# Kernel optimization log

Measured on AMD Instinct MI355X. Metric: run time of the kernel, lower is better.

Reference implementation:

```python
import jax, jax.numpy as jnp
import numpy as np

CODEBOOK_DIM = 12          # log2(codebook_size)
CODEBOOK_SIZE = 4096
DIM = 512
INV_TEMPERATURE = 100.0
CODEBOOK_SCALE = 1.0
DIVERSITY_GAMMA = 1.0
ENTROPY_LOSS_WEIGHT = 0.1
EPS = 1e-5


def setup_inputs() -> dict:
    key = jax.random.key(0)
    k_x, k_wi, k_wo = jax.random.split(key, 3)
    x = jax.random.normal(k_x, (4, 4096, DIM), dtype=jnp.float32)
    # nn.Linear weights: (out_features, in_features)
    w_in = jax.random.normal(k_wi, (CODEBOOK_DIM, DIM), dtype=jnp.float32) * 0.02
    b_in = jnp.zeros((CODEBOOK_DIM,), dtype=jnp.float32)
    w_out = jax.random.normal(k_wo, (DIM, CODEBOOK_DIM), dtype=jnp.float32) * 0.02
    b_out = jnp.zeros((DIM,), dtype=jnp.float32)
    return {"x": x, "w_in": w_in, "b_in": b_in, "w_out": w_out, "b_out": b_out}


def _entropy(prob):
    return (-prob * jnp.log(jnp.clip(prob, EPS))).sum(axis=-1)


def _make_codebook():
    mask = (2 ** jnp.arange(CODEBOOK_DIM - 1, -1, -1)).astype(jnp.int32)  # [d]
    all_codes = jnp.arange(CODEBOOK_SIZE, dtype=jnp.int32)
    bits = ((all_codes[:, None] & mask) != 0).astype(jnp.float32)  # [cs, d]
    codebook = bits * CODEBOOK_SCALE * 2 - CODEBOOK_SCALE  # {-1, +1}
    return mask, codebook


def reference(x, w_in, b_in, w_out, b_out):
    mask, codebook = _make_codebook()

    # project in: [b, n, dim] -> [b, n, d]
    xp = jnp.einsum('bnd,cd->bnc', x, w_in) + b_in  # c == codebook_dim here

    # sign quantization (num_codebooks = 1, so c-dim is implicit)
    quantized = jnp.where(xp > 0, CODEBOOK_SCALE, -CODEBOOK_SCALE).astype(xp.dtype)
    indices = ((quantized > 0).astype(jnp.int32) * mask).sum(axis=-1)  # [b, n]

    # straight-through estimator (training path)
    x_st = xp + jax.lax.stop_gradient(quantized - xp)

    # entropy aux loss over full codebook (frac_per_sample_entropy = 1.0)
    flat = xp.reshape(-1, CODEBOOK_DIM)  # original (pre-quant) input, [bn, d]
    # -distance * inv_temp = 2 * inv_temp * <x, code>
    logits = (2.0 * INV_TEMPERATURE) * (flat @ codebook.T)  # [bn, cs]
    prob = jax.nn.softmax(logits, axis=-1)
    per_sample_entropy = _entropy(prob).mean()
    avg_prob = prob.mean(axis=0)  # [cs]
    codebook_entropy = _entropy(avg_prob)
    entropy_aux_loss = per_sample_entropy - DIVERSITY_GAMMA * codebook_entropy
    aux_loss = entropy_aux_loss * ENTROPY_LOSS_WEIGHT

    # project out: [b, n, d] -> [b, n, dim]
    out = jnp.einsum('bnc,dc->bnd', x_st, w_out) + b_out
    return out, indices, aux_loss
```

## Files before the change

### kernel.cpp

```cpp
#include <hip/hip_runtime.h>
#include <hip/hip_bf16.h>


#define NS    16384
#define NOUT  (NS*512)
#define AUXO  (NOUT+NS)
#define INVT2 200.0f
#define NBLK  512

__global__ __launch_bounds__(512, 4) void k_main(
    const float* __restrict__ x,
    const float* __restrict__ w_in,  const float* __restrict__ b_in,
    const float* __restrict__ w_out, const float* __restrict__ b_out,
    float* __restrict__ out, float* __restrict__ idx_out,
    float* __restrict__ P, float* __restrict__ Csum) {

  __shared__ float s_wi[6144];
  __shared__ float s_wt[6144];
  __shared__ float s_phi[32][64];
  __shared__ float s_psi[32][64];
  __shared__ float s_xp[8][4][12];
  __shared__ float s_h[8];

  const int t = threadIdx.x;

  for (int k = 0; k < 12; ++k) {
    int f  = t + k * 512;
    int kk = f & 3;
    int q  = f >> 2;
    int sub = q & 15, e4 = (q >> 4) & 7, d = q >> 7;
    int e  = sub * 32 + e4 * 4 + kk;
    s_wi[f] = w_in[d * 512 + e];
    s_wt[f] = w_out[t * 12 + k];
  }
  __syncthreads();

  const int wave = t >> 6, lane = t & 63;
  const int g = lane >> 4, sub = lane & 15;

  float bin[12];
  #pragma unroll
  for (int d = 0; d < 12; ++d) bin[d] = b_in[d];

  const int i0 = blockIdx.x * 32 + wave * 4 + g;

  const float4* xr0 = (const float4*)(x + (size_t)i0 * 512 + sub * 32);
  float4 xv0[8];
  #pragma unroll
  for (int e4 = 0; e4 < 8; ++e4) xv0[e4] = xr0[e4];

  float p0[12];
  #pragma unroll
  for (int d = 0; d < 12; ++d) p0[d] = 0.f;
  #pragma unroll
  for (int e4 = 0; e4 < 8; ++e4) {
    #pragma unroll
    for (int d = 0; d < 12; ++d) {
      float4 w4 = ((const float4*)s_wi)[d * 128 + e4 * 16 + sub];
      p0[d] += xv0[e4].x * w4.x + xv0[e4].y * w4.y + xv0[e4].z * w4.z + xv0[e4].w * w4.w;
    }
  }
  #pragma unroll
  for (int d = 0; d < 12; ++d) {
    #pragma unroll
    for (int m = 1; m <= 8; m <<= 1) {
      p0[d] += __shfl_xor(p0[d], m, 16);
    }
    p0[d] += bin[d];
  }

  unsigned idx0 = 0u;
  #pragma unroll
  for (int d = 0; d < 12; ++d) {
    idx0 |= (p0[d] > 0.f ? 1u : 0u) << (11 - d);
  }
  if (sub == 0) {
    idx_out[i0] = (float)idx0;
    #pragma unroll
    for (int d = 0; d < 12; ++d) s_xp[wave][g][d] = p0[d];
  }

  float sg0[12];
  #pragma unroll
  for (int d = 0; d < 12; ++d) sg0[d] = p0[d] > 0.f ? 1.f : -1.f;

  float4* or0 = (float4*)(out + (size_t)i0 * 512);
  #pragma unroll
  for (int e4 = 0; e4 < 8; ++e4) {
    float4 bo = ((const float4*)b_out)[e4 * 16 + sub];
    float4 o0 = bo;
    #pragma unroll
    for (int d = 0; d < 12; ++d) {
      float4 w4 = ((const float4*)s_wt)[d * 128 + e4 * 16 + sub];
      o0.x += sg0[d] * w4.x; o0.y += sg0[d] * w4.y; o0.z += sg0[d] * w4.z; o0.w += sg0[d] * w4.w;
    }
    or0[e4 * 16 + sub] = o0;
  }

  float hacc = 0.f;
  #pragma unroll 1
  for (int s = 0; s < 4; ++s) {
    float xq[12];
    #pragma unroll
    for (int d = 0; d < 12; ++d) xq[d] = s_xp[wave][s][d];

    float hi = 0.f, lo = 0.f, ah = 0.f, al = 0.f;
    #pragma unroll
    for (int d = 0; d < 6; ++d) {
      int bh = (lane >> (5 - d)) & 1;
      hi += bh ? xq[d]     : -xq[d];
      lo += bh ? xq[6 + d] : -xq[6 + d];
      ah += fabsf(xq[d]);
      al += fabsf(xq[6 + d]);
    }
    float lhi = INVT2 * (hi - ah);
    float llo = INVT2 * (lo - al);
    float ehi = __expf(lhi);
    float elo = __expf(llo);
    float Shi = ehi, Slo = elo;
    #pragma unroll
    for (int m = 1; m <= 32; m <<= 1) {
      Shi += __shfl_xor(Shi, m);
      Slo += __shfl_xor(Slo, m);
    }
    float phi = ehi / Shi;
    float psi = elo / Slo;
    float lnShi = __logf(Shi), lnSlo = __logf(Slo);
    hacc += phi * (lhi - lnShi) + psi * (llo - lnSlo);

    const int ws = wave * 4 + s;
    s_phi[ws][lane] = phi;
    s_psi[ws][lane] = psi;
  }

  #pragma unroll
  for (int m = 1; m <= 32; m <<= 1) hacc += __shfl_xor(hacc, m);
  if (lane == 0) s_h[wave] = hacc;
  __syncthreads();
  if (t == 0) {
    float hs = 0.f;
    for (int w2 = 0; w2 < 8; ++w2) hs += s_h[w2];
    atomicAdd(Csum, hs);
  }

  const int jb = (t >> 5) * 4;
  const int lb = (t & 31) * 2;
  float a00 = 0.f, a01 = 0.f, a10 = 0.f, a11 = 0.f;
  float a20 = 0.f, a21 = 0.f, a30 = 0.f, a31 = 0.f;
  #pragma unroll 4
  for (int s = 0; s < 32; ++s) {
    float4 ph = *(const float4*)&s_phi[s][jb];
    float2 ps = *(const float2*)&s_psi[s][lb];
    a00 += ph.x * ps.x; a01 += ph.x * ps.y;
    a10 += ph.y * ps.x; a11 += ph.y * ps.y;
    a20 += ph.z * ps.x; a21 += ph.z * ps.y;
    a30 += ph.w * ps.x; a31 += ph.w * ps.y;
  }
  float* Pr = P + (size_t)blockIdx.x * 4096;
  *(float2*)&Pr[(jb + 0) * 64 + lb] = make_float2(a00, a01);
  *(float2*)&Pr[(jb + 1) * 64 + lb] = make_float2(a10, a11);
  *(float2*)&Pr[(jb + 2) * 64 + lb] = make_float2(a20, a21);
  *(float2*)&Pr[(jb + 3) * 64 + lb] = make_float2(a30, a31);
}

__global__ __launch_bounds__(256) void k_reduce(const float* __restrict__ P,
                                                float* __restrict__ Esum) {
  __shared__ float red[16][17];
  __shared__ float ered[16];
  const int t = threadIdx.x;
  const int cl = t & 15, rg = t >> 4;
  const int c = blockIdx.x * 16 + cl;
  float s = 0.f;
  #pragma unroll
  for (int k = 0; k < 32; ++k) s += P[(size_t)(rg + k * 16) * 4096 + c];
  red[rg][cl] = s;
  __syncthreads();
  if (t < 16) {
    float tot = 0.f;
    #pragma unroll
    for (int r = 0; r < 16; ++r) tot += red[r][t];
    float pb = tot * (1.f / (float)NS);
    ered[t] = pb * __logf(fmaxf(pb, 1e-5f));
  }
  __syncthreads();
  if (t == 0) {
    float e = 0.f;
    #pragma unroll
    for (int r = 0; r < 16; ++r) e += ered[r];
    atomicAdd(Esum, e);
  }
}

__global__ void k_final(const float* __restrict__ Csum, const float* __restrict__ Esum,
                        float* __restrict__ aux) {
  if (threadIdx.x == 0) {
    float per_sample_entropy = -Csum[0] * (1.f / (float)NS);
    float codebook_entropy   = -Esum[0];
    aux[0] = 0.1f * (per_sample_entropy - codebook_entropy);
  }
}

extern "C" void kernel_launch(void* const* d_in, const int* in_sizes, int n_in,
                              void* d_out, int out_size, void* d_ws, size_t ws_size,
                              hipStream_t stream) {
  const float* x     = (const float*)d_in[0];
  const float* w_in  = (const float*)d_in[1];
  const float* b_in  = (const float*)d_in[2];
  const float* w_out = (const float*)d_in[3];
  const float* b_out = (const float*)d_in[4];
  float* out = (float*)d_out;

  float* P    = (float*)d_ws;
  float* scal = (float*)((char*)d_ws + (size_t)NBLK * 4096 * 4);

  hipMemsetAsync(scal, 0, 2 * sizeof(float), stream);
  k_main<<<NBLK, 512, 0, stream>>>(x, w_in, b_in, w_out, b_out,
                                   out, out + NOUT, P, scal);
  k_reduce<<<256, 256, 0, stream>>>(P, scal + 1);
  k_final<<<1, 64, 0, stream>>>(scal, scal + 1, out + AUXO);
}
```

Measured before the change: 113.9 us.

## Precompute 4096-code output table and gather rows; fold final kernel into reduce

Because the straight-through output depends only on the 12 sign bits, a new kernel builds a 4096x512 table of w_out·sign(code)+b_out, and the main kernel copies the row for each token's index instead of doing the 12-term FMA projection. This also drops the shared-memory w_out staging from the main kernel, freeing LDS. Separately, the final aux-loss kernel is folded into the reduce kernel through a last-block counter. The cost is an 8 MB table write plus gathered reads, which may or may not stay in cache, and one extra launch.

```diff
diff --git a/kernel.cpp b/kernel.cpp
--- a/kernel.cpp
+++ b/kernel.cpp
@@ -8,15 +8,43 @@
 #define INVT2 200.0f
 #define NBLK  512
 
+__global__ __launch_bounds__(512) void k_table(const float* __restrict__ w_out,
+                                               const float* __restrict__ b_out,
+                                               float* __restrict__ T) {
+  __shared__ float s_wt[6144];
+  const int t = threadIdx.x;
+  #pragma unroll
+  for (int k = 0; k < 12; ++k) s_wt[t + k * 512] = w_out[t * 12 + k];
+  __syncthreads();
+
+  const int c = blockIdx.x * 16 + (t >> 5);
+  float sg[12];
+  #pragma unroll
+  for (int d = 0; d < 12; ++d) sg[d] = ((c >> (11 - d)) & 1) ? 1.f : -1.f;
+
+  float4* Trow = (float4*)(T + (size_t)c * 512);
+  #pragma unroll
+  for (int k4 = 0; k4 < 4; ++k4) {
+    const int m = (t & 31) + k4 * 32;
+    float4 bo = ((const float4*)b_out)[m];
+    float4 o = bo;
+    #pragma unroll
+    for (int d = 0; d < 12; ++d) {
+      float4 w4 = ((const float4*)s_wt)[d * 128 + m];
+      o.x += sg[d] * w4.x; o.y += sg[d] * w4.y; o.z += sg[d] * w4.z; o.w += sg[d] * w4.w;
+    }
+    Trow[m] = o;
+  }
+}
+
 __global__ __launch_bounds__(512, 4) void k_main(
     const float* __restrict__ x,
     const float* __restrict__ w_in,  const float* __restrict__ b_in,
-    const float* __restrict__ w_out, const float* __restrict__ b_out,
+    const float* __restrict__ T,
     float* __restrict__ out, float* __restrict__ idx_out,
     float* __restrict__ P, float* __restrict__ Csum) {
 
   __shared__ float s_wi[6144];
-  __shared__ float s_wt[6144];
   __shared__ float s_phi[32][64];
   __shared__ float s_psi[32][64];
   __shared__ float s_xp[8][4][12];
@@ -24,6 +52,7 @@
 
   const int t = threadIdx.x;
 
+  #pragma unroll
   for (int k = 0; k < 12; ++k) {
     int f  = t + k * 512;
     int kk = f & 3;
@@ -31,7 +60,6 @@
     int sub = q & 15, e4 = (q >> 4) & 7, d = q >> 7;
     int e  = sub * 32 + e4 * 4 + kk;
     s_wi[f] = w_in[d * 512 + e];
-    s_wt[f] = w_out[t * 12 + k];
   }
   __syncthreads();
 
@@ -80,21 +108,13 @@
     for (int d = 0; d < 12; ++d) s_xp[wave][g][d] = p0[d];
   }
 
-  float sg0[12];
-  #pragma unroll
-  for (int d = 0; d < 12; ++d) sg0[d] = p0[d] > 0.f ? 1.f : -1.f;
-
-  float4* or0 = (float4*)(out + (size_t)i0 * 512);
-  #pragma unroll
-  for (int e4 = 0; e4 < 8; ++e4) {
-    float4 bo = ((const float4*)b_out)[e4 * 16 + sub];
-    float4 o0 = bo;
-    #pragma unroll
-    for (int d = 0; d < 12; ++d) {
-      float4 w4 = ((const float4*)s_wt)[d * 128 + e4 * 16 + sub];
-      o0.x += sg0[d] * w4.x; o0.y += sg0[d] * w4.y; o0.z += sg0[d] * w4.z; o0.w += sg0[d] * w4.w;
-    }
-    or0[e4 * 16 + sub] = o0;
+  {
+    const float4* Trow = (const float4*)(T + (size_t)idx0 * 512);
+    float4* or0 = (float4*)(out + (size_t)i0 * 512);
+    #pragma unroll
+    for (int e4 = 0; e4 < 8; ++e4) {
+      or0[e4 * 16 + sub] = Trow[e4 * 16 + sub];
+    }
   }
 
   float hacc = 0.f;
@@ -164,7 +184,8 @@
 }
 
 __global__ __launch_bounds__(256) void k_reduce(const float* __restrict__ P,
-                                                float* __restrict__ Esum) {
+                                                float* __restrict__ scal,
+                                                float* __restrict__ aux) {
   __shared__ float red[16][17];
   __shared__ float ered[16];
   const int t = threadIdx.x;
@@ -187,16 +208,16 @@
     float e = 0.f;
     #pragma unroll
     for (int r = 0; r < 16; ++r) e += ered[r];
-    atomicAdd(Esum, e);
-  }
-}
-
-__global__ void k_final(const float* __restrict__ Csum, const float* __restrict__ Esum,
-                        float* __restrict__ aux) {
-  if (threadIdx.x == 0) {
-    float per_sample_entropy = -Csum[0] * (1.f / (float)NS);
-    float codebook_entropy   = -Esum[0];
-    aux[0] = 0.1f * (per_sample_entropy - codebook_entropy);
+    atomicAdd(&scal[1], e);
+    __threadfence();
+    unsigned done = atomicAdd((unsigned*)&scal[2], 1u);
+    if (done == 255u) {
+      float E = atomicAdd(&scal[1], 0.f);
+      float C = atomicAdd(&scal[0], 0.f);
+      float per_sample_entropy = -C * (1.f / (float)NS);
+      float codebook_entropy   = -E;
+      aux[0] = 0.1f * (per_sample_entropy - codebook_entropy);
+    }
   }
 }
 
@@ -210,12 +231,13 @@
   const float* b_out = (const float*)d_in[4];
   float* out = (float*)d_out;
 
-  float* P    = (float*)d_ws;
-  float* scal = (float*)((char*)d_ws + (size_t)NBLK * 4096 * 4);
-
-  hipMemsetAsync(scal, 0, 2 * sizeof(float), stream);
-  k_main<<<NBLK, 512, 0, stream>>>(x, w_in, b_in, w_out, b_out,
+  float* T    = (float*)d_ws;
+  float* P    = T + (size_t)4096 * 512;
+  float* scal = P + (size_t)NBLK * 4096;
+
+  hipMemsetAsync(scal, 0, 3 * sizeof(float), stream);
+  k_table<<<256, 512, 0, stream>>>(w_out, b_out, T);
+  k_main<<<NBLK, 512, 0, stream>>>(x, w_in, b_in, T,
                                    out, out + NOUT, P, scal);
-  k_reduce<<<256, 256, 0, stream>>>(P, scal + 1);
-  k_final<<<1, 64, 0, stream>>>(scal, scal + 1, out + AUXO);
-}
+  k_reduce<<<256, 256, 0, stream>>>(P, scal, out + AUXO);
+}
```

Measured after the change: 120.2 us. 1.06x slower.

## Read weights directly from global/L1 instead of LDS staging; fold final kernel into reduce

Applied to the files above, without the earlier changes.

Drops the per-block LDS staging of w_in and w_out (48 KB of shared memory) and the block barrier that follows it. Weights are now read directly from global memory through cache, with the output projection restructured to read w_out rows as contiguous float4s. The lower shared memory use could raise occupancy, but every thread now issues more global and L1 loads. Separately, k_final is removed: the last k_reduce block, found with an atomic counter, computes aux, which saves one kernel launch.

```diff
diff --git a/kernel.cpp b/kernel.cpp
--- a/kernel.cpp
+++ b/kernel.cpp
@@ -15,29 +15,19 @@
     float* __restrict__ out, float* __restrict__ idx_out,
     float* __restrict__ P, float* __restrict__ Csum) {
 
-  __shared__ float s_wi[6144];
-  __shared__ float s_wt[6144];
   __shared__ float s_phi[32][64];
   __shared__ float s_psi[32][64];
   __shared__ float s_xp[8][4][12];
   __shared__ float s_h[8];
 
   const int t = threadIdx.x;
-
-  for (int k = 0; k < 12; ++k) {
-    int f  = t + k * 512;
-    int kk = f & 3;
-    int q  = f >> 2;
-    int sub = q & 15, e4 = (q >> 4) & 7, d = q >> 7;
-    int e  = sub * 32 + e4 * 4 + kk;
-    s_wi[f] = w_in[d * 512 + e];
-    s_wt[f] = w_out[t * 12 + k];
-  }
-  __syncthreads();
-
   const int wave = t >> 6, lane = t & 63;
   const int g = lane >> 4, sub = lane & 15;
 
+  const float4* wi4 = (const float4*)w_in;
+  const float4* wo4 = (const float4*)w_out;
+  const float4* bo4 = (const float4*)b_out;
+
   float bin[12];
   #pragma unroll
   for (int d = 0; d < 12; ++d) bin[d] = b_in[d];
@@ -56,7 +46,7 @@
   for (int e4 = 0; e4 < 8; ++e4) {
     #pragma unroll
     for (int d = 0; d < 12; ++d) {
-      float4 w4 = ((const float4*)s_wi)[d * 128 + e4 * 16 + sub];
+      float4 w4 = wi4[d * 128 + sub * 8 + e4];
       p0[d] += xv0[e4].x * w4.x + xv0[e4].y * w4.y + xv0[e4].z * w4.z + xv0[e4].w * w4.w;
     }
   }
@@ -87,14 +77,34 @@
   float4* or0 = (float4*)(out + (size_t)i0 * 512);
   #pragma unroll
   for (int e4 = 0; e4 < 8; ++e4) {
-    float4 bo = ((const float4*)b_out)[e4 * 16 + sub];
-    float4 o0 = bo;
-    #pragma unroll
-    for (int d = 0; d < 12; ++d) {
-      float4 w4 = ((const float4*)s_wt)[d * 128 + e4 * 16 + sub];
-      o0.x += sg0[d] * w4.x; o0.y += sg0[d] * w4.y; o0.z += sg0[d] * w4.z; o0.w += sg0[d] * w4.w;
-    }
-    or0[e4 * 16 + sub] = o0;
+    const int M = e4 * 16 + sub;
+    const float4* wr = wo4 + 12 * M;
+    float4 o = bo4[M];
+    {
+      float4 a = wr[0], b = wr[1], c = wr[2];
+      o.x += sg0[0]*a.x; o.x += sg0[1]*a.y; o.x += sg0[2]*a.z; o.x += sg0[3]*a.w;
+      o.x += sg0[4]*b.x; o.x += sg0[5]*b.y; o.x += sg0[6]*b.z; o.x += sg0[7]*b.w;
+      o.x += sg0[8]*c.x; o.x += sg0[9]*c.y; o.x += sg0[10]*c.z; o.x += sg0[11]*c.w;
+    }
+    {
+      float4 a = wr[3], b = wr[4], c = wr[5];
+      o.y += sg0[0]*a.x; o.y += sg0[1]*a.y; o.y += sg0[2]*a.z; o.y += sg0[3]*a.w;
+      o.y += sg0[4]*b.x; o.y += sg0[5]*b.y; o.y += sg0[6]*b.z; o.y += sg0[7]*b.w;
+      o.y += sg0[8]*c.x; o.y += sg0[9]*c.y; o.y += sg0[10]*c.z; o.y += sg0[11]*c.w;
+    }
+    {
+      float4 a = wr[6], b = wr[7], c = wr[8];
+      o.z += sg0[0]*a.x; o.z += sg0[1]*a.y; o.z += sg0[2]*a.z; o.z += sg0[3]*a.w;
+      o.z += sg0[4]*b.x; o.z += sg0[5]*b.y; o.z += sg0[6]*b.z; o.z += sg0[7]*b.w;
+      o.z += sg0[8]*c.x; o.z += sg0[9]*c.y; o.z += sg0[10]*c.z; o.z += sg0[11]*c.w;
+    }
+    {
+      float4 a = wr[9], b = wr[10], c = wr[11];
+      o.w += sg0[0]*a.x; o.w += sg0[1]*a.y; o.w += sg0[2]*a.z; o.w += sg0[3]*a.w;
+      o.w += sg0[4]*b.x; o.w += sg0[5]*b.y; o.w += sg0[6]*b.z; o.w += sg0[7]*b.w;
+      o.w += sg0[8]*c.x; o.w += sg0[9]*c.y; o.w += sg0[10]*c.z; o.w += sg0[11]*c.w;
+    }
+    or0[M] = o;
   }
 
   float hacc = 0.f;
@@ -164,7 +174,8 @@
 }
 
 __global__ __launch_bounds__(256) void k_reduce(const float* __restrict__ P,
-                                                float* __restrict__ Esum) {
+                                                float* __restrict__ scal,
+                                                float* __restrict__ aux) {
   __shared__ float red[16][17];
   __shared__ float ered[16];
   const int t = threadIdx.x;
@@ -187,16 +198,16 @@
     float e = 0.f;
     #pragma unroll
     for (int r = 0; r < 16; ++r) e += ered[r];
-    atomicAdd(Esum, e);
-  }
-}
-
-__global__ void k_final(const float* __restrict__ Csum, const float* __restrict__ Esum,
-                        float* __restrict__ aux) {
-  if (threadIdx.x == 0) {
-    float per_sample_entropy = -Csum[0] * (1.f / (float)NS);
-    float codebook_entropy   = -Esum[0];
-    aux[0] = 0.1f * (per_sample_entropy - codebook_entropy);
+    atomicAdd(&scal[1], e);
+    __threadfence();
+    unsigned done = atomicAdd((unsigned*)&scal[2], 1u);
+    if (done == 255u) {
+      float E = atomicAdd(&scal[1], 0.f);
+      float C = atomicAdd(&scal[0], 0.f);
+      float per_sample_entropy = -C * (1.f / (float)NS);
+      float codebook_entropy   = -E;
+      aux[0] = 0.1f * (per_sample_entropy - codebook_entropy);
+    }
   }
 }
 
@@ -211,11 +222,10 @@
   float* out = (float*)d_out;
 
   float* P    = (float*)d_ws;
-  float* scal = (float*)((char*)d_ws + (size_t)NBLK * 4096 * 4);
-
-  hipMemsetAsync(scal, 0, 2 * sizeof(float), stream);
+  float* scal = P + (size_t)NBLK * 4096;
+
+  hipMemsetAsync(scal, 0, 3 * sizeof(float), stream);
   k_main<<<NBLK, 512, 0, stream>>>(x, w_in, b_in, w_out, b_out,
                                    out, out + NOUT, P, scal);
-  k_reduce<<<256, 256, 0, stream>>>(P, scal + 1);
-  k_final<<<1, 64, 0, stream>>>(scal, scal + 1, out + AUXO);
+  k_reduce<<<256, 256, 0, stream>>>(P, scal, out + AUXO);
 }
```

Result: slower. 177.7 us (+56.0%).

## Drop memset and final kernel; fold finalisation into reduce via last-block counter

Applied to the files above, without the earlier changes.

Removes the hipMemsetAsync and the single-thread final kernel. Block 0 of the main kernel now zeroes the scalars, per-block entropy partials are written to a buffer instead of atomics, and the reduce kernel (now 64 blocks with 64 columns each) sums them. The last reduce block, found through an atomic counter, computes the aux loss. This saves two launches per call, at the cost of fewer, longer reduce blocks and an atomic completion protocol.

```diff
diff --git a/kernel.cpp b/kernel.cpp
--- a/kernel.cpp
+++ b/kernel.cpp
@@ -7,13 +7,14 @@
 #define AUXO  (NOUT+NS)
 #define INVT2 200.0f
 #define NBLK  512
+#define RBLK  64
 
 __global__ __launch_bounds__(512, 4) void k_main(
     const float* __restrict__ x,
     const float* __restrict__ w_in,  const float* __restrict__ b_in,
     const float* __restrict__ w_out, const float* __restrict__ b_out,
     float* __restrict__ out, float* __restrict__ idx_out,
-    float* __restrict__ P, float* __restrict__ Csum) {
+    float* __restrict__ P, float* __restrict__ Hpart, float* __restrict__ scal) {
 
   __shared__ float s_wi[6144];
   __shared__ float s_wt[6144];
@@ -33,6 +34,9 @@
     s_wi[f] = w_in[d * 512 + e];
     s_wt[f] = w_out[t * 12 + k];
   }
+  if (blockIdx.x == 0 && t == 0) {
+    scal[0] = 0.f; scal[1] = 0.f; ((unsigned*)scal)[2] = 0u;
+  }
   __syncthreads();
 
   const int wave = t >> 6, lane = t & 63;
@@ -140,7 +144,7 @@
   if (t == 0) {
     float hs = 0.f;
     for (int w2 = 0; w2 < 8; ++w2) hs += s_h[w2];
-    atomicAdd(Csum, hs);
+    Hpart[blockIdx.x] = hs;
   }
 
   const int jb = (t >> 5) * 4;
@@ -164,39 +168,43 @@
 }
 
 __global__ __launch_bounds__(256) void k_reduce(const float* __restrict__ P,
-                                                float* __restrict__ Esum) {
-  __shared__ float red[16][17];
-  __shared__ float ered[16];
+                                                const float* __restrict__ Hpart,
+                                                float* __restrict__ scal,
+                                                float* __restrict__ aux) {
+  __shared__ float red[4][64];
   const int t = threadIdx.x;
-  const int cl = t & 15, rg = t >> 4;
-  const int c = blockIdx.x * 16 + cl;
+  const int c = blockIdx.x * 64 + (t & 63);
+  const int rg = t >> 6;
   float s = 0.f;
-  #pragma unroll
-  for (int k = 0; k < 32; ++k) s += P[(size_t)(rg + k * 16) * 4096 + c];
-  red[rg][cl] = s;
-  __syncthreads();
-  if (t < 16) {
-    float tot = 0.f;
-    #pragma unroll
-    for (int r = 0; r < 16; ++r) tot += red[r][t];
+  #pragma unroll 8
+  for (int j = 0; j < 128; ++j) s += P[(size_t)(rg * 128 + j) * 4096 + c];
+  red[rg][t & 63] = s;
+  __syncthreads();
+  if (t < 64) {
+    float tot = (red[0][t] + red[1][t]) + (red[2][t] + red[3][t]);
     float pb = tot * (1.f / (float)NS);
-    ered[t] = pb * __logf(fmaxf(pb, 1e-5f));
-  }
-  __syncthreads();
+    float e = pb * __logf(fmaxf(pb, 1e-5f));
+    #pragma unroll
+    for (int m = 1; m <= 32; m <<= 1) e += __shfl_xor(e, m);
+    if (t == 0) atomicAdd(&scal[1], e);
+  }
+  if (t == 128) {
+    float ch = 0.f;
+    #pragma unroll
+    for (int k = 0; k < 8; ++k) ch += Hpart[blockIdx.x * 8 + k];
+    atomicAdd(&scal[0], ch);
+  }
+  __syncthreads();
+  __threadfence();
   if (t == 0) {
-    float e = 0.f;
-    #pragma unroll
-    for (int r = 0; r < 16; ++r) e += ered[r];
-    atomicAdd(Esum, e);
-  }
-}
-
-__global__ void k_final(const float* __restrict__ Csum, const float* __restrict__ Esum,
-                        float* __restrict__ aux) {
-  if (threadIdx.x == 0) {
-    float per_sample_entropy = -Csum[0] * (1.f / (float)NS);
-    float codebook_entropy   = -Esum[0];
-    aux[0] = 0.1f * (per_sample_entropy - codebook_entropy);
+    unsigned done = atomicAdd((unsigned*)&scal[2], 1u);
+    if (done == RBLK - 1) {
+      float E = atomicAdd(&scal[1], 0.f);
+      float C = atomicAdd(&scal[0], 0.f);
+      float per_sample_entropy = -C * (1.f / (float)NS);
+      float codebook_entropy   = -E;
+      aux[0] = 0.1f * (per_sample_entropy - codebook_entropy);
+    }
   }
 }
 
@@ -210,12 +218,11 @@
   const float* b_out = (const float*)d_in[4];
   float* out = (float*)d_out;
 
-  float* P    = (float*)d_ws;
-  float* scal = (float*)((char*)d_ws + (size_t)NBLK * 4096 * 4);
-
-  hipMemsetAsync(scal, 0, 2 * sizeof(float), stream);
+  float* P     = (float*)d_ws;
+  float* Hpart = P + (size_t)NBLK * 4096;
+  float* scal  = Hpart + NBLK;
+
   k_main<<<NBLK, 512, 0, stream>>>(x, w_in, b_in, w_out, b_out,
-                                   out, out + NOUT, P, scal);
-  k_reduce<<<256, 256, 0, stream>>>(P, scal + 1);
-  k_final<<<1, 64, 0, stream>>>(scal, scal + 1, out + AUXO);
+                                   out, out + NOUT, P, Hpart, scal);
+  k_reduce<<<RBLK, 256, 0, stream>>>(P, Hpart, scal, out + AUXO);
 }
```

New measurement: 116.8 us. 2.6% more time.
